# Performance work log

Measured on AMD Instinct MI355X. Metric: run time of the kernel, lower is better.

## Reference

```python
import jax, jax.numpy as jnp
import numpy as np

N_NODES = 100000
N_EDGES = 1600000
NUM_RELS = 200
NUM_BASES = 4
IN_FEAT = 20   # hardcoded by `view(-1, 1, 20)` in the torch source
OUT_FEAT = 20
SUBMAT_IN = IN_FEAT // NUM_BASES   # 5
SUBMAT_OUT = OUT_FEAT // NUM_BASES # 5


def setup_inputs() -> dict:
    key = jax.random.key(0)
    ks = jax.random.split(key, 9)
    return {
        "h": jax.random.normal(ks[0], (N_NODES, IN_FEAT), dtype=jnp.float32),
        "weight": jax.random.normal(ks[1], (NUM_RELS, NUM_BASES * SUBMAT_IN * SUBMAT_OUT), dtype=jnp.float32),
        "bias_term": jax.random.normal(ks[2], (NUM_RELS, OUT_FEAT), dtype=jnp.float32),
        "gate_weight": jax.random.normal(ks[3], (NUM_RELS, OUT_FEAT, 1), dtype=jnp.float32),
        "gate_bias": jax.random.normal(ks[4], (NUM_RELS, 1), dtype=jnp.float32),
        "loop_weight": jax.random.normal(ks[5], (IN_FEAT, OUT_FEAT), dtype=jnp.float32),
        "edge_src": jax.random.randint(ks[6], (N_EDGES,), 0, N_NODES, dtype=jnp.int32),
        "edge_dst": jax.random.randint(ks[7], (N_EDGES,), 0, N_NODES, dtype=jnp.int32),
        "etype": jax.random.randint(ks[8], (NUM_RELS,), 0, NUM_RELS, dtype=jnp.int32) if False else jax.random.randint(ks[8], (N_EDGES,), 0, NUM_RELS, dtype=jnp.int32),
    }


def reference(h, weight, bias_term, gate_weight, gate_bias, loop_weight, edge_src, edge_dst, etype):
    n_nodes = h.shape[0]
    # self-loop message (dropout=0.0 -> identity)
    loop_message = h @ loop_weight                                    # [N, out]
    # per-edge relation-indexed gathers
    W = weight[etype].reshape(-1, NUM_BASES, SUBMAT_IN, SUBMAT_OUT)   # [E, B, si, so]
    src = h[edge_src]                                                 # [E, in]
    node = src.reshape(-1, NUM_BASES, SUBMAT_IN)                      # [E, B, si]
    # block-diagonal small matmul
    msg = jnp.einsum('ebi,ebio->ebo', node, W).reshape(-1, OUT_FEAT)  # [E, out]
    # gate: sigmoid(<full src node, gate_weight_r> + gate_bias_r)
    gw = gate_weight[etype, :, 0]                                     # [E, out(=20=in)]
    gb = gate_bias[etype, 0]                                          # [E]
    gate = jax.nn.sigmoid(jnp.sum(src * gw, axis=-1) + gb)            # [E]
    msg = gate[:, None] * (msg + bias_term[etype])                    # [E, out]
    # scatter-sum aggregation to destination nodes (zero init for isolated nodes)
    agg = jax.ops.segment_sum(msg, edge_dst, num_segments=n_nodes)    # [N, out]
    return jax.nn.relu(agg + loop_message)
```

## Files before the change

### kernel.cpp

```cpp
#include <hip/hip_runtime.h>
#include <hip/hip_fp16.h>
#include <math.h>

#define IN_FEAT 20
#define OUT_FEAT 20
#define NUM_BASES 4
#define SUBMAT_IN 5
#define SUBMAT_OUT 5
#define NUM_RELS 200
#define CAP 64
#define NPB 160
#define BCAP 3072
#define EPB 4096


__global__ void __launch_bounds__(256)
hpad_zero_kernel(const float* __restrict__ h, __half* __restrict__ h_pad,
                 int* __restrict__ cursor, int n_nodes, int nb) {
    int v = blockIdx.x * 256 + threadIdx.x;
    if (v < nb) cursor[v] = 0;
    if (v >= n_nodes) return;
    const float4* hp = (const float4*)(h + (size_t)v * IN_FEAT);
    float4 a = hp[0], b = hp[1], c = hp[2], d = hp[3], e = hp[4];
    __half2 p0 = __floats2half2_rn(a.x, a.y), p1 = __floats2half2_rn(a.z, a.w);
    __half2 p2 = __floats2half2_rn(b.x, b.y), p3 = __floats2half2_rn(b.z, b.w);
    __half2 p4 = __floats2half2_rn(c.x, c.y), p5 = __floats2half2_rn(c.z, c.w);
    __half2 p6 = __floats2half2_rn(d.x, d.y), p7 = __floats2half2_rn(d.z, d.w);
    __half2 p8 = __floats2half2_rn(e.x, e.y), p9 = __floats2half2_rn(e.z, e.w);
    uint4 w0, w1; uint2 w2;
    w0.x = *(unsigned*)&p0; w0.y = *(unsigned*)&p1; w0.z = *(unsigned*)&p2; w0.w = *(unsigned*)&p3;
    w1.x = *(unsigned*)&p4; w1.y = *(unsigned*)&p5; w1.z = *(unsigned*)&p6; w1.w = *(unsigned*)&p7;
    w2.x = *(unsigned*)&p8; w2.y = *(unsigned*)&p9;
    char* dst = (char*)(h_pad + (size_t)v * 32);
    *(uint4*)(dst)      = w0;
    *(uint4*)(dst + 16) = w1;
    *(uint2*)(dst + 32) = w2;
}

__global__ void __launch_bounds__(1024)
bucket_scatter_kernel(const int* __restrict__ edge_src,
                      const int* __restrict__ edge_dst,
                      const int* __restrict__ etype,
                      int* __restrict__ cursor,
                      int2* __restrict__ bucketed,
                      int n_edges, int nb) {
    __shared__ int  lhist[640];
    __shared__ int  lofs[640];
    __shared__ int  lrank[640];
    __shared__ int  lbase[640];
    __shared__ int2 img[EPB];
    int tid = threadIdx.x;
    for (int i = tid; i < nb; i += 1024) { lhist[i] = 0; lrank[i] = 0; }
    __syncthreads();

    int blockbase = blockIdx.x * EPB;
    int e0 = blockbase + tid * 4;
    int s[4], d[4], t[4], bk[4];
    bool val[4];
    if (e0 + 3 < n_edges) {
        int4 sv = *(const int4*)(edge_src + e0);
        int4 dv = *(const int4*)(edge_dst + e0);
        int4 tv = *(const int4*)(etype + e0);
        s[0]=sv.x; s[1]=sv.y; s[2]=sv.z; s[3]=sv.w;
        d[0]=dv.x; d[1]=dv.y; d[2]=dv.z; d[3]=dv.w;
        t[0]=tv.x; t[1]=tv.y; t[2]=tv.z; t[3]=tv.w;
        val[0]=val[1]=val[2]=val[3]=true;
    } else {
#pragma unroll
        for (int k = 0; k < 4; ++k) {
            int e = e0 + k;
            val[k] = (e < n_edges);
            s[k] = val[k] ? edge_src[e] : 0;
            d[k] = val[k] ? edge_dst[e] : 0;
            t[k] = val[k] ? etype[e] : 0;
        }
    }
#pragma unroll
    for (int k = 0; k < 4; ++k) {
        bk[k] = d[k] / NPB;
        if (val[k]) atomicAdd(&lhist[bk[k]], 1);
    }
    __syncthreads();

    if (tid < nb) lofs[tid] = lhist[tid];
    __syncthreads();
    for (int step = 1; step < nb; step <<= 1) {
        int v2 = (tid < nb && tid >= step) ? lofs[tid - step] : 0;
        __syncthreads();
        if (tid < nb && tid >= step) lofs[tid] += v2;
        __syncthreads();
    }
    if (tid < nb) {
        lofs[tid] -= lhist[tid];
        if (lhist[tid] > 0) lbase[tid] = atomicAdd(&cursor[tid], lhist[tid]);
    }
    __syncthreads();

#pragma unroll
    for (int k = 0; k < 4; ++k) {
        if (val[k]) {
            int r = atomicAdd(&lrank[bk[k]], 1);
            unsigned packed = (unsigned)s[k] | ((unsigned)t[k] << 17);
            img[lofs[bk[k]] + r] = make_int2(d[k], (int)packed);
        }
    }
    __syncthreads();

    int m = n_edges - blockbase; if (m > EPB) m = EPB;
    for (int i = tid; i < m; i += 1024) {
        int2 e = img[i];
        int b2 = e.x / NPB;
        int dst = lbase[b2] + (i - lofs[b2]);
        if (dst < BCAP) bucketed[(size_t)b2 * BCAP + dst] = e;
    }
}

__global__ void __launch_bounds__(1024)
bucket_scan_kernel(const int* __restrict__ cursor, int* __restrict__ bucket_base,
                   int nb) {
    __shared__ int s[1024];
    int tid = threadIdx.x;
    int v = (tid < nb) ? min(cursor[tid], BCAP) : 0;
    s[tid] = v;
    __syncthreads();
    for (int step = 1; step < 1024; step <<= 1) {
        int t = (tid >= step) ? s[tid - step] : 0;
        __syncthreads();
        if (tid >= step) s[tid] += t;
        __syncthreads();
    }
    if (tid < nb) bucket_base[tid] = s[tid] - v;
}

__global__ void __launch_bounds__(1024)
place_csr_kernel(const int* __restrict__ cursor,
                 const int* __restrict__ bucket_base,
                 const int2* __restrict__ bucketed,
                 unsigned* __restrict__ records,
                 int* __restrict__ cnt,
                 int* __restrict__ off,
                 int n_nodes) {
    __shared__ int lcnt[NPB];
    __shared__ int sscan[NPB];
    __shared__ int lrank[NPB];
    int b = blockIdx.x, tid = threadIdx.x;
    int node0 = b * NPB;
    if (tid < NPB) { lcnt[tid] = 0; lrank[tid] = 0; }
    __syncthreads();
    int m = cursor[b]; if (m > BCAP) m = BCAP;
    int gbase = bucket_base[b];

    for (int i = tid; i < m; i += 1024) {
        int2 r = bucketed[(size_t)b * BCAP + i];
        atomicAdd(&lcnt[r.x - node0], 1);
    }
    __syncthreads();
    if (tid < NPB) sscan[tid] = lcnt[tid];
    __syncthreads();
    for (int step = 1; step < NPB; step <<= 1) {
        int t = (tid < NPB && tid >= step) ? sscan[tid - step] : 0;
        __syncthreads();
        if (tid < NPB && tid >= step) sscan[tid] += t;
        __syncthreads();
    }
    if (tid < NPB) {
        int excl = sscan[tid] - lcnt[tid];
        int v = node0 + tid;
        if (v < n_nodes) { cnt[v] = lcnt[tid]; off[v] = gbase + excl; }
        sscan[tid] = excl;
    }
    __syncthreads();
    for (int i = tid; i < m; i += 1024) {
        int2 r = bucketed[(size_t)b * BCAP + i];
        int dl = r.x - node0;
        int rk = atomicAdd(&lrank[dl], 1);
        records[(size_t)gbase + sscan[dl] + rk] = (unsigned)r.y;
    }
}

__global__ void __launch_bounds__(1024, 4)
gather_kernel(const float* __restrict__ h,
              const __half* __restrict__ h_pad,
              const float* __restrict__ loop_weight,
              const float* __restrict__ weight,
              const float* __restrict__ bias_term,
              const float* __restrict__ gate_weight,
              const float* __restrict__ gate_bias,
              const int* __restrict__ cnt,
              const int* __restrict__ off,
              const unsigned* __restrict__ records,
              float* __restrict__ out, int n_nodes, int n_groups) {
    __shared__ __half2 lds_wp[NUM_RELS * 51];
    __shared__ float   lds_gwt[IN_FEAT * NUM_RELS];
    __shared__ float   lds_gb[NUM_RELS];
    __shared__ float   lds_lw[IN_FEAT * OUT_FEAT];
    int tid = threadIdx.x;
    for (int idx = tid; idx < NUM_RELS * 50; idx += 1024) {
        int t = idx / 50, f = idx - t * 50;
        lds_wp[t * 51 + f] = __floats2half2_rn(weight[t * 100 + f],
                                               weight[t * 100 + f + 50]);
    }
    for (int idx = tid; idx < IN_FEAT * NUM_RELS; idx += 1024) {
        int t = idx / IN_FEAT, i = idx - t * IN_FEAT;
        lds_gwt[i * NUM_RELS + t] = gate_weight[idx];
    }
    for (int idx = tid; idx < NUM_RELS; idx += 1024) lds_gb[idx] = gate_bias[idx];
    for (int idx = tid; idx < IN_FEAT * OUT_FEAT; idx += 1024) lds_lw[idx] = loop_weight[idx];
    __syncthreads();

    int wave = blockIdx.x * 16 + (tid >> 6);
    int nwaves = gridDim.x * 16;
    int l = tid & 63;
    int l16 = l & 15;

    for (int grp = wave; grp < n_groups; grp += nwaves) {
        int v = grp * 4 + (l >> 4);
        bool valid = (v < n_nodes);
        int c = 0, base = 0;
        if (valid) { c = cnt[v]; base = off[v]; }
        if (c > CAP) c = CAP;

        float acc[OUT_FEAT];
#pragma unroll
        for (int j = 0; j < OUT_FEAT; ++j) acc[j] = 0.0f;

        if (valid) {
#pragma unroll
            for (int i0 = 0; i0 < 2; ++i0) {
                int i = l16 + i0 * 16;
                if (i < IN_FEAT) {
                    float s = h[(size_t)v * IN_FEAT + i];
#pragma unroll
                    for (int j = 0; j < OUT_FEAT; ++j)
                        acc[j] = fmaf(s, lds_lw[i * OUT_FEAT + j], acc[j]);
                }
            }
        }

#pragma unroll
        for (int it = 0; it < 4; ++it) {
            int slot = l16 + it * 16;
            if (valid && slot < c) {
                unsigned p = records[(size_t)base + slot];
                int srcid = (int)(p & 0x1FFFFu);
                int t = (int)(p >> 17);

                const char* sp = (const char*)(h_pad + (size_t)srcid * 32);
                uint4 A = *(const uint4*)(sp);
                uint4 B = *(const uint4*)(sp + 16);
                uint2 C = *(const uint2*)(sp + 32);
                float src[IN_FEAT];
                {
                    unsigned u[10] = {A.x, A.y, A.z, A.w, B.x, B.y, B.z, B.w, C.x, C.y};
#pragma unroll
                    for (int q = 0; q < 10; ++q) {
                        __half2 hv = *reinterpret_cast<__half2*>(&u[q]);
                        float2 f = __half22float2(hv);
                        src[2 * q] = f.x; src[2 * q + 1] = f.y;
                    }
                }

                float g = lds_gb[t];
#pragma unroll
                for (int i = 0; i < IN_FEAT; ++i)
                    g = fmaf(src[i], lds_gwt[i * NUM_RELS + t], g);
                g = 1.0f / (1.0f + __expf(-g));

#pragma unroll
                for (int i = 0; i < IN_FEAT; ++i) src[i] *= g;

                const __half2* wp = lds_wp + t * 51;
#pragma unroll
                for (int f = 0; f < 50; ++f) {
                    float2 w = __half22float2(wp[f]);
                    const int b0 = f / 25, r = f - b0 * 25;
                    const int i0 = r / 5, o0 = r - i0 * 5;
                    acc[b0 * 5 + o0] =
                        fmaf(src[b0 * 5 + i0], w.x, acc[b0 * 5 + o0]);
                    acc[(b0 + 2) * 5 + o0] =
                        fmaf(src[(b0 + 2) * 5 + i0], w.y, acc[(b0 + 2) * 5 + o0]);
                }

                const float4* btp = (const float4*)(bias_term + (size_t)t * OUT_FEAT);
#pragma unroll
                for (int k = 0; k < OUT_FEAT / 4; ++k) {
                    float4 bv = btp[k];
                    acc[4 * k + 0] = fmaf(g, bv.x, acc[4 * k + 0]);
                    acc[4 * k + 1] = fmaf(g, bv.y, acc[4 * k + 1]);
                    acc[4 * k + 2] = fmaf(g, bv.z, acc[4 * k + 2]);
                    acc[4 * k + 3] = fmaf(g, bv.w, acc[4 * k + 3]);
                }
            }
        }

#pragma unroll
        for (int mask = 8; mask > 0; mask >>= 1) {
#pragma unroll
            for (int j = 0; j < OUT_FEAT; ++j)
                acc[j] += __shfl_xor(acc[j], mask, 16);
        }

        if (valid && l16 < OUT_FEAT / 4) {
            float4 tv;
            tv.x = fmaxf(acc[4 * l16 + 0], 0.0f);
            tv.y = fmaxf(acc[4 * l16 + 1], 0.0f);
            tv.z = fmaxf(acc[4 * l16 + 2], 0.0f);
            tv.w = fmaxf(acc[4 * l16 + 3], 0.0f);
            ((float4*)(out + (size_t)v * OUT_FEAT))[l16] = tv;
        }
    }
}

__global__ void loop_msg_kernel(const float* __restrict__ h,
                                const float* __restrict__ loop_weight,
                                float* __restrict__ out, int n_nodes) {
    int v = blockIdx.x * blockDim.x + threadIdx.x;
    if (v >= n_nodes) return;
    float src[IN_FEAT];
    const float4* hp = (const float4*)(h + (size_t)v * IN_FEAT);
#pragma unroll
    for (int i = 0; i < IN_FEAT / 4; ++i) {
        float4 t = hp[i];
        src[4 * i + 0] = t.x; src[4 * i + 1] = t.y;
        src[4 * i + 2] = t.z; src[4 * i + 3] = t.w;
    }
    float acc[OUT_FEAT];
#pragma unroll
    for (int j = 0; j < OUT_FEAT; ++j) acc[j] = 0.0f;
#pragma unroll
    for (int i = 0; i < IN_FEAT; ++i) {
        float s = src[i];
#pragma unroll
        for (int j = 0; j < OUT_FEAT; ++j)
            acc[j] = fmaf(s, loop_weight[i * OUT_FEAT + j], acc[j]);
    }
    float4* op = (float4*)(out + (size_t)v * OUT_FEAT);
#pragma unroll
    for (int j = 0; j < OUT_FEAT / 4; ++j) {
        float4 t;
        t.x = acc[4 * j + 0]; t.y = acc[4 * j + 1];
        t.z = acc[4 * j + 2]; t.w = acc[4 * j + 3];
        op[j] = t;
    }
}

__global__ void edge_atomic_kernel(const float* __restrict__ h,
                                   const float* __restrict__ weight,
                                   const float* __restrict__ bias_term,
                                   const float* __restrict__ gate_weight,
                                   const float* __restrict__ gate_bias,
                                   const int* __restrict__ edge_src,
                                   const int* __restrict__ edge_dst,
                                   const int* __restrict__ etype,
                                   float* __restrict__ out, int n_edges) {
    int e = blockIdx.x * blockDim.x + threadIdx.x;
    if (e >= n_edges) return;
    int s = edge_src[e], d = edge_dst[e], t = etype[e];
    float src[IN_FEAT];
    const float4* hp = (const float4*)(h + (size_t)s * IN_FEAT);
#pragma unroll
    for (int i = 0; i < IN_FEAT / 4; ++i) {
        float4 v = hp[i];
        src[4 * i + 0] = v.x; src[4 * i + 1] = v.y;
        src[4 * i + 2] = v.z; src[4 * i + 3] = v.w;
    }
    const float* W = weight + (size_t)t * 100;
    float msg[OUT_FEAT];
#pragma unroll
    for (int j = 0; j < OUT_FEAT; ++j) msg[j] = 0.0f;
#pragma unroll
    for (int b = 0; b < NUM_BASES; ++b)
#pragma unroll
        for (int i = 0; i < SUBMAT_IN; ++i) {
            float sv = src[b * SUBMAT_IN + i];
#pragma unroll
            for (int o = 0; o < SUBMAT_OUT; ++o)
                msg[b * SUBMAT_OUT + o] =
                    fmaf(sv, W[(b * SUBMAT_IN + i) * SUBMAT_OUT + o],
                         msg[b * SUBMAT_OUT + o]);
        }
    const float* gw = gate_weight + (size_t)t * OUT_FEAT;
    float g = gate_bias[t];
#pragma unroll
    for (int i = 0; i < IN_FEAT; ++i) g = fmaf(src[i], gw[i], g);
    g = 1.0f / (1.0f + __expf(-g));
    const float* bt = bias_term + (size_t)t * OUT_FEAT;
    float* dstp = out + (size_t)d * OUT_FEAT;
#pragma unroll
    for (int j = 0; j < OUT_FEAT; ++j) atomicAdd(&dstp[j], g * (msg[j] + bt[j]));
}

__global__ void relu_kernel(float* __restrict__ out, int n4) {
    int i = blockIdx.x * blockDim.x + threadIdx.x;
    if (i >= n4) return;
    float4* p = (float4*)out;
    float4 v = p[i];
    v.x = fmaxf(v.x, 0.0f); v.y = fmaxf(v.y, 0.0f);
    v.z = fmaxf(v.z, 0.0f); v.w = fmaxf(v.w, 0.0f);
    p[i] = v;
}

extern "C" void kernel_launch(void* const* d_in, const int* in_sizes, int n_in,
                              void* d_out, int out_size, void* d_ws, size_t ws_size,
                              hipStream_t stream) {
    const float* h           = (const float*)d_in[0];
    const float* weight      = (const float*)d_in[1];
    const float* bias_term   = (const float*)d_in[2];
    const float* gate_weight = (const float*)d_in[3];
    const float* gate_bias   = (const float*)d_in[4];
    const float* loop_weight = (const float*)d_in[5];
    const int* edge_src      = (const int*)d_in[6];
    const int* edge_dst      = (const int*)d_in[7];
    const int* etype         = (const int*)d_in[8];
    float* out = (float*)d_out;

    const int n_nodes = in_sizes[0] / IN_FEAT;
    const int n_edges = in_sizes[6];
    const int nb = (n_nodes + NPB - 1) / NPB;

    size_t off_cursor   = 0;
    size_t off_bbase    = (((size_t)nb * 4 + 127) / 128) * 128;
    size_t off_bucketed = ((off_bbase + (size_t)nb * 4 + 127) / 128) * 128;
    size_t off_records  = ((off_bucketed + (size_t)nb * BCAP * 8 + 127) / 128) * 128;
    size_t off_cnt      = ((off_records + (size_t)n_edges * 4 + 127) / 128) * 128;
    size_t off_offs     = ((off_cnt + (size_t)n_nodes * 4 + 127) / 128) * 128;
    size_t off_hpad     = ((off_offs + (size_t)n_nodes * 4 + 127) / 128) * 128;
    size_t need = off_hpad + (size_t)n_nodes * 64;

    bool ok = (ws_size >= need) && (n_nodes <= (1 << 17)) && (nb <= 1024) &&
              (in_sizes[4] == NUM_RELS) && (in_sizes[1] == NUM_RELS * 100) &&
              (in_sizes[5] == IN_FEAT * OUT_FEAT);

    if (ok) {
        int*  cursor      = (int*)((char*)d_ws + off_cursor);
        int*  bucket_base = (int*)((char*)d_ws + off_bbase);
        int2* bucketed    = (int2*)((char*)d_ws + off_bucketed);
        unsigned* records = (unsigned*)((char*)d_ws + off_records);
        int*  cnt         = (int*)((char*)d_ws + off_cnt);
        int*  off         = (int*)((char*)d_ws + off_offs);
        __half* h_pad     = (__half*)((char*)d_ws + off_hpad);

        hpad_zero_kernel<<<(n_nodes + 255) / 256, 256, 0, stream>>>(
            h, h_pad, cursor, n_nodes, nb);
        bucket_scatter_kernel<<<(n_edges + EPB - 1) / EPB, 1024, 0, stream>>>(
            edge_src, edge_dst, etype, cursor, bucketed, n_edges, nb);
        bucket_scan_kernel<<<1, 1024, 0, stream>>>(cursor, bucket_base, nb);
        place_csr_kernel<<<nb, 1024, 0, stream>>>(
            cursor, bucket_base, bucketed, records, cnt, off, n_nodes);
        int n_groups = (n_nodes + 3) / 4;
        gather_kernel<<<512, 1024, 0, stream>>>(
            h, h_pad, loop_weight, weight, bias_term, gate_weight, gate_bias,
            cnt, off, records, out, n_nodes, n_groups);
    } else {
        loop_msg_kernel<<<(n_nodes + 255) / 256, 256, 0, stream>>>(
            h, loop_weight, out, n_nodes);
        edge_atomic_kernel<<<(n_edges + 255) / 256, 256, 0, stream>>>(
            h, weight, bias_term, gate_weight, gate_bias,
            edge_src, edge_dst, etype, out, n_edges);
        relu_kernel<<<(n_nodes * OUT_FEAT / 4 + 255) / 256, 256, 0, stream>>>(
            out, n_nodes * OUT_FEAT / 4);
    }
}
```

Measured before the change: 201.1 us.

## Fuse bucket scan into CSR placement and stage gate/bias params as half2 in LDS

Removes the separate single-block bucket_scan launch. Each place_csr block now computes its own bucket base with a shared-memory reduction over the preceding bucket counts, which saves one kernel launch and its dependency at the cost of redundant reduction work per block. In the gather kernel, gate weights and bias_term are packed as half2 into LDS with a padded stride, replacing float LDS reads and global float4 bias loads. This lowers per-edge memory traffic but adds fp16 rounding to the gate and bias values.

After: 227.5 us. +13.1%, slower.

```diff
diff --git a/kernel.cpp b/kernel.cpp
--- a/kernel.cpp
+++ b/kernel.cpp
@@ -116,39 +116,29 @@
 }
 
 __global__ void __launch_bounds__(1024)
-bucket_scan_kernel(const int* __restrict__ cursor, int* __restrict__ bucket_base,
-                   int nb) {
-    __shared__ int s[1024];
-    int tid = threadIdx.x;
-    int v = (tid < nb) ? min(cursor[tid], BCAP) : 0;
-    s[tid] = v;
-    __syncthreads();
-    for (int step = 1; step < 1024; step <<= 1) {
-        int t = (tid >= step) ? s[tid - step] : 0;
-        __syncthreads();
-        if (tid >= step) s[tid] += t;
-        __syncthreads();
-    }
-    if (tid < nb) bucket_base[tid] = s[tid] - v;
-}
-
-__global__ void __launch_bounds__(1024)
 place_csr_kernel(const int* __restrict__ cursor,
-                 const int* __restrict__ bucket_base,
                  const int2* __restrict__ bucketed,
                  unsigned* __restrict__ records,
                  int* __restrict__ cnt,
                  int* __restrict__ off,
-                 int n_nodes) {
+                 int n_nodes, int nb) {
+    __shared__ int red[1024];
     __shared__ int lcnt[NPB];
     __shared__ int sscan[NPB];
     __shared__ int lrank[NPB];
     int b = blockIdx.x, tid = threadIdx.x;
     int node0 = b * NPB;
+
+    red[tid] = (tid < b && tid < nb) ? min(cursor[tid], BCAP) : 0;
     if (tid < NPB) { lcnt[tid] = 0; lrank[tid] = 0; }
     __syncthreads();
+    for (int step = 512; step > 0; step >>= 1) {
+        if (tid < step) red[tid] += red[tid + step];
+        __syncthreads();
+    }
+    int gbase = red[0];
+
     int m = cursor[b]; if (m > BCAP) m = BCAP;
-    int gbase = bucket_base[b];
 
     for (int i = tid; i < m; i += 1024) {
         int2 r = bucketed[(size_t)b * BCAP + i];
@@ -191,7 +181,8 @@
               const unsigned* __restrict__ records,
               float* __restrict__ out, int n_nodes, int n_groups) {
     __shared__ __half2 lds_wp[NUM_RELS * 51];
-    __shared__ float   lds_gwt[IN_FEAT * NUM_RELS];
+    __shared__ __half2 lds_gw2[10 * 201];
+    __shared__ __half2 lds_bt2[10 * 201];
     __shared__ float   lds_gb[NUM_RELS];
     __shared__ float   lds_lw[IN_FEAT * OUT_FEAT];
     int tid = threadIdx.x;
@@ -200,9 +191,12 @@
         lds_wp[t * 51 + f] = __floats2half2_rn(weight[t * 100 + f],
                                                weight[t * 100 + f + 50]);
     }
-    for (int idx = tid; idx < IN_FEAT * NUM_RELS; idx += 1024) {
-        int t = idx / IN_FEAT, i = idx - t * IN_FEAT;
-        lds_gwt[i * NUM_RELS + t] = gate_weight[idx];
+    for (int idx = tid; idx < 10 * NUM_RELS; idx += 1024) {
+        int p = idx / NUM_RELS, t = idx - p * NUM_RELS;
+        lds_gw2[p * 201 + t] = __floats2half2_rn(gate_weight[t * IN_FEAT + p],
+                                                 gate_weight[t * IN_FEAT + p + 10]);
+        lds_bt2[p * 201 + t] = __floats2half2_rn(bias_term[t * OUT_FEAT + p],
+                                                 bias_term[t * OUT_FEAT + p + 10]);
     }
     for (int idx = tid; idx < NUM_RELS; idx += 1024) lds_gb[idx] = gate_bias[idx];
     for (int idx = tid; idx < IN_FEAT * OUT_FEAT; idx += 1024) lds_lw[idx] = loop_weight[idx];
@@ -261,9 +255,12 @@
                 }
 
                 float g = lds_gb[t];
-#pragma unroll
-                for (int i = 0; i < IN_FEAT; ++i)
-                    g = fmaf(src[i], lds_gwt[i * NUM_RELS + t], g);
+                const __half2* gwp = lds_gw2 + t;
+#pragma unroll
+                for (int p2 = 0; p2 < 10; ++p2) {
+                    float2 w = __half22float2(gwp[p2 * 201]);
+                    g = fmaf(src[p2], w.x, fmaf(src[p2 + 10], w.y, g));
+                }
                 g = 1.0f / (1.0f + __expf(-g));
 
 #pragma unroll
@@ -281,14 +278,12 @@
                         fmaf(src[(b0 + 2) * 5 + i0], w.y, acc[(b0 + 2) * 5 + o0]);
                 }
 
-                const float4* btp = (const float4*)(bias_term + (size_t)t * OUT_FEAT);
-#pragma unroll
-                for (int k = 0; k < OUT_FEAT / 4; ++k) {
-                    float4 bv = btp[k];
-                    acc[4 * k + 0] = fmaf(g, bv.x, acc[4 * k + 0]);
-                    acc[4 * k + 1] = fmaf(g, bv.y, acc[4 * k + 1]);
-                    acc[4 * k + 2] = fmaf(g, bv.z, acc[4 * k + 2]);
-                    acc[4 * k + 3] = fmaf(g, bv.w, acc[4 * k + 3]);
+                const __half2* btp2 = lds_bt2 + t;
+#pragma unroll
+                for (int p2 = 0; p2 < 10; ++p2) {
+                    float2 bv = __half22float2(btp2[p2 * 201]);
+                    acc[p2]      = fmaf(g, bv.x, acc[p2]);
+                    acc[p2 + 10] = fmaf(g, bv.y, acc[p2 + 10]);
                 }
             }
         }
@@ -419,8 +414,7 @@
     const int nb = (n_nodes + NPB - 1) / NPB;
 
     size_t off_cursor   = 0;
-    size_t off_bbase    = (((size_t)nb * 4 + 127) / 128) * 128;
-    size_t off_bucketed = ((off_bbase + (size_t)nb * 4 + 127) / 128) * 128;
+    size_t off_bucketed = (((size_t)nb * 4 + 127) / 128) * 128;
     size_t off_records  = ((off_bucketed + (size_t)nb * BCAP * 8 + 127) / 128) * 128;
     size_t off_cnt      = ((off_records + (size_t)n_edges * 4 + 127) / 128) * 128;
     size_t off_offs     = ((off_cnt + (size_t)n_nodes * 4 + 127) / 128) * 128;
@@ -433,7 +427,6 @@
 
     if (ok) {
         int*  cursor      = (int*)((char*)d_ws + off_cursor);
-        int*  bucket_base = (int*)((char*)d_ws + off_bbase);
         int2* bucketed    = (int2*)((char*)d_ws + off_bucketed);
         unsigned* records = (unsigned*)((char*)d_ws + off_records);
         int*  cnt         = (int*)((char*)d_ws + off_cnt);
@@ -444,9 +437,8 @@
             h, h_pad, cursor, n_nodes, nb);
         bucket_scatter_kernel<<<(n_edges + EPB - 1) / EPB, 1024, 0, stream>>>(
             edge_src, edge_dst, etype, cursor, bucketed, n_edges, nb);
-        bucket_scan_kernel<<<1, 1024, 0, stream>>>(cursor, bucket_base, nb);
         place_csr_kernel<<<nb, 1024, 0, stream>>>(
-            cursor, bucket_base, bucketed, records, cnt, off, n_nodes);
+            cursor, bucketed, records, cnt, off, n_nodes, nb);
         int n_groups = (n_nodes + 3) / 4;
         gather_kernel<<<512, 1024, 0, stream>>>(
             h, h_pad, loop_weight, weight, bias_term, gate_weight, gate_bias,
```
